# Performance work log

Measured on AMD Instinct MI355X. Metric: run time of the kernel, lower is better.

Reference implementation:

```python
import jax, jax.numpy as jnp
import numpy as np

B, L_Q, L_K, H, D = 8, 2048, 2048, 8, 64
FACTOR = 5
U_PART = max(1, min(FACTOR * int(np.ceil(np.log(L_K + 1))), L_K))  # sample_k = 40
U_TOP = max(1, min(FACTOR * int(np.ceil(np.log(L_Q + 1))), L_Q))   # n_top = 40


def setup_inputs() -> dict:
    key = jax.random.key(0)
    kq, kk, kv, ki = jax.random.split(key, 4)
    queries = jax.random.normal(kq, (B, L_Q, H, D), dtype=jnp.float32)
    keys = jax.random.normal(kk, (B, L_K, H, D), dtype=jnp.float32)
    values = jax.random.normal(kv, (B, L_K, H, D), dtype=jnp.float32)
    # random key-sampling indices (GPU randint in the torch module), shared across B,H
    index_sample = jax.random.randint(ki, (L_Q, U_PART), 0, L_K)
    return {"queries": queries, "keys": keys, "values": values,
            "index_sample": index_sample}


def reference(queries, keys, values, index_sample):
    b, l_q, h, d = queries.shape
    l_k = keys.shape[1]
    # [B, L, H, D] -> [B, H, L, D]
    Q = jnp.transpose(queries, (0, 2, 1, 3))
    K = jnp.transpose(keys, (0, 2, 1, 3))
    V = jnp.transpose(values, (0, 2, 1, 3))

    # --- _prob_QK: sparse sampling + sparsity-measure topk query selection ---
    K_sample = K[:, :, index_sample, :]                     # [B,H,L_Q,S,D]
    Q_K_sample = jnp.einsum('bhqe,bhqse->bhqs', Q, K_sample)
    M = Q_K_sample.max(axis=-1) - Q_K_sample.mean(axis=-1)  # [B,H,L_Q]
    _, M_top = jax.lax.top_k(M, U_TOP)                      # [B,H,u] query indices
    Q_reduce = jnp.take_along_axis(Q, M_top[..., None], axis=2)  # [B,H,u,D]
    scores = jnp.einsum('bhue,bhke->bhuk', Q_reduce, K)     # [B,H,u,L_K]
    scores = scores * (1.0 / np.sqrt(d))

    # --- causal mask for selected queries (mask_flag=True) ---
    key_pos = jnp.arange(l_k)
    causal = key_pos[None, None, None, :] > M_top[..., None]  # key > query pos
    scores = jnp.where(causal, -jnp.inf, scores)

    attn = jax.nn.softmax(scores, axis=-1)                  # dropout in eval mode
    attn_out = jnp.einsum('bhuk,bhkd->bhud', attn, V)       # [B,H,u,D]

    # --- initial context (causal => cumulative sum of V) + scatter update ---
    context = jnp.cumsum(V, axis=2)                         # [B,H,L_Q,D]
    b_idx = jnp.arange(b)[:, None, None]
    h_idx = jnp.arange(h)[None, :, None]
    context = context.at[b_idx, h_idx, M_top].set(attn_out)

    return jnp.transpose(context, (0, 2, 1, 3))             # [B,L_Q,H,D]
```

## Files before the change

### kernel.cpp

```cpp
#include <hip/hip_runtime.h>
#include <math.h>

#define Bb 8
#define Hh 8
#define LQ 2048
#define LK 2048
#define Dd 64
#define Uu 40
#define NCH 64
#define CHUNK (LK / NCH)
#define NSPL 8
#define CK (LK / NSPL)
#define SM_BLOCKS (Bb * (LQ / 8))
#define PART_BLOCKS (Bb * NCH / 2)
#define ATTN_BLOCKS (Bb * Hh * NSPL)
#define SCAN_BLOCKS (Bb * NCH / 2)

typedef float f32x4 __attribute__((ext_vector_type(4)));
typedef short bf16x8 __attribute__((ext_vector_type(8)));

__device__ __forceinline__ short f2bf(float x) {
    unsigned u = __float_as_uint(x);
    unsigned r = u + 0x7fffu + ((u >> 16) & 1u);
    return (short)(r >> 16);
}

__device__ __forceinline__ bf16x8 pack8(float4 a, float4 b) {
    bf16x8 r;
    r[0] = f2bf(a.x); r[1] = f2bf(a.y); r[2] = f2bf(a.z); r[3] = f2bf(a.w);
    r[4] = f2bf(b.x); r[5] = f2bf(b.y); r[6] = f2bf(b.z); r[7] = f2bf(b.w);
    return r;
}

__global__ __launch_bounds__(256) void k_main(
    const float* __restrict__ Qp, const float* __restrict__ Kp,
    const int* __restrict__ idxs, const float* __restrict__ Vp,
    float* __restrict__ M, float* __restrict__ part)
{
    int t = threadIdx.x;

    if (blockIdx.x >= SM_BLOCKS) {
        int bid2 = blockIdx.x - SM_BLOCKS;
        int b = bid2 >> 5;
        int c = (bid2 & 31) * 2 + (t >> 7);
        int h = (t >> 4) & 7, d4 = (t & 15) * 4;

        const float* vb = Vp + ((size_t)(b * LK + c * CHUNK)) * 512 + h * 64 + d4;
        float4 s = make_float4(0.f, 0.f, 0.f, 0.f);
#pragma unroll 4
        for (int l = 0; l < CHUNK; ++l) {
            float4 v = *reinterpret_cast<const float4*>(vb + (size_t)l * 512);
            s.x += v.x; s.y += v.y; s.z += v.z; s.w += v.w;
        }
        int bh = b * 8 + h;
        *reinterpret_cast<float4*>(&part[(size_t)(bh * NCH + c) * Dd + d4]) = s;
        return;
    }

    int b  = blockIdx.x & 7;
    int qt = blockIdx.x >> 3;
    int lane = t & 63, wave = t >> 6;

    __shared__ int sIdx[8 * Uu];
    for (int i = t; i < 8 * Uu; i += 256)
        sIdx[i] = idxs[(qt * 8) * Uu + i];
    __syncthreads();

    const size_t HD = 512;
    const float* Kb = Kp + (size_t)b * LK * HD + lane * 4;

#pragma unroll
    for (int i = 0; i < 2; ++i) {
        int lq = wave * 2 + i;
        int q  = qt * 8 + lq;
        const int* sI = &sIdx[lq * Uu];
#pragma unroll
        for (int ph = 0; ph < 2; ++ph) {
            f32x4 qa = __builtin_nontemporal_load(
                reinterpret_cast<const f32x4*>(
                    Qp + ((size_t)b * LQ + q) * HD + ph * 256) + lane);

            float mx = -INFINITY, sm = 0.f;
#pragma unroll 8
            for (int s = 0; s < Uu; ++s) {
                int kidx = sI[s];
                f32x4 kv = *reinterpret_cast<const f32x4*>(
                    Kb + (size_t)kidx * HD + ph * 256);
                float p = qa[0] * kv[0] + qa[1] * kv[1]
                        + qa[2] * kv[2] + qa[3] * kv[3];
                p += __shfl_xor(p, 1, 64);
                p += __shfl_xor(p, 2, 64);
                p += __shfl_xor(p, 4, 64);
                p += __shfl_xor(p, 8, 64);
                mx = fmaxf(mx, p); sm += p;
            }
            if ((lane & 15) == 0) {
                int h = ph * 4 + (lane >> 4);
                __builtin_nontemporal_store(
                    mx - sm * (1.0f / Uu), &M[((b * 8 + h) << 11) + q]);
            }
        }
    }
}

__global__ __launch_bounds__(64) void k_topk(
    const float* __restrict__ M, int* __restrict__ Mtop)
{
    int bh = blockIdx.x;
    int lane = threadIdx.x;
    __shared__ float Ml[LQ];

    for (int j = lane; j < LQ; j += 64)
        Ml[j] = M[bh * LQ + j];
    __syncthreads();

    float lv = -INFINITY; int li = LQ;
    for (int j = 0; j < 32; ++j) {
        int idx = lane + 64 * j;
        float x = Ml[idx];
        if (x > lv) { lv = x; li = idx; }
    }

    int myp = 0;
    for (int u = 0; u < Uu; ++u) {
        float v = lv; int id = li;
#pragma unroll
        for (int off = 32; off > 0; off >>= 1) {
            float ov = __shfl_xor(v, off, 64);
            int   oi = __shfl_xor(id, off, 64);
            if (ov > v || (ov == v && oi < id)) { v = ov; id = oi; }
        }
        if (u == lane) myp = id;
        if ((id & 63) == lane) {
            Ml[id] = -INFINITY;
            lv = -INFINITY; li = LQ;
            for (int j = 0; j < 32; ++j) {
                int idx = lane + 64 * j;
                float x = Ml[idx];
                if (x > lv) { lv = x; li = idx; }
            }
        }
    }

    int rank = 0;
    for (int j = 0; j < Uu; ++j) {
        int pj = __shfl(myp, j, 64);
        rank += (pj < myp && lane < Uu) ? 1 : 0;
    }
    if (lane < Uu) Mtop[bh * Uu + rank] = myp;
}

__global__ __launch_bounds__(256) void k_attn_scan(
    const float* __restrict__ Qp, const float* __restrict__ Kp,
    const float* __restrict__ Vp, const int* __restrict__ Mtop,
    const float* __restrict__ part, float* __restrict__ pacc,
    float* __restrict__ pl, float* __restrict__ out)
{
    int t = threadIdx.x;

    if (blockIdx.x >= ATTN_BLOCKS) {
        int bid2 = blockIdx.x - ATTN_BLOCKS;
        int b = bid2 >> 5;
        int ch = (bid2 & 31) * 2 + (t >> 7);
        int t2 = t & 127;
        int h = t2 >> 4, d4 = (t2 & 15) * 4;
        int bh = b * 8 + h;

        float4 run = make_float4(0.f, 0.f, 0.f, 0.f);
        for (int cc = 0; cc < ch; ++cc) {
            float4 p4 = *reinterpret_cast<const float4*>(
                &part[(size_t)(bh * NCH + cc) * Dd + d4]);
            run.x += p4.x; run.y += p4.y; run.z += p4.z; run.w += p4.w;
        }

        int l0 = ch * CHUNK;
        const float* vb = Vp + ((size_t)(b * LK + l0)) * 512 + h * 64 + d4;
        float* ob = out + ((size_t)(b * LQ + l0)) * 512 + h * 64 + d4;
#pragma unroll 4
        for (int l = 0; l < CHUNK; ++l) {
            float4 v = *reinterpret_cast<const float4*>(vb + (size_t)l * 512);
            run.x += v.x; run.y += v.y; run.z += v.z; run.w += v.w;
            *reinterpret_cast<float4*>(ob + (size_t)l * 512) = run;
        }
        return;
    }

    int bh = blockIdx.x >> 3;
    int c  = blockIdx.x & (NSPL - 1);
    int b = bh >> 3, h = bh & 7;
    int lane = t & 63, w = t >> 6;
    int col = lane & 15, hi = lane >> 4;

    __shared__ int sP[48];
    __shared__ __align__(16) short sPl[2][48][80];
    __shared__ float sL[4][48];

    if (t < 48) sP[t] = (t < Uu) ? Mtop[bh * Uu + t] : -1;
    __syncthreads();

    const int pmax = sP[Uu - 1];
    const int qmax0 = sP[15], qmax1 = sP[31];

    bf16x8 qf[3][2];
#pragma unroll
    for (int qb = 0; qb < 3; ++qb) {
        int q = qb * 16 + col;
        int row = sP[q];
#pragma unroll
        for (int ks = 0; ks < 2; ++ks) {
            const float* qp = Qp + (((size_t)b * LQ + max(row, 0)) * Hh + h) * Dd
                              + ks * 32 + hi * 8;
            float4 x = *reinterpret_cast<const float4*>(qp);
            float4 y = *reinterpret_cast<const float4*>(qp + 4);
            bf16x8 f = pack8(x, y);
            if (row < 0) f = (bf16x8)(short)0;
            qf[qb][ks] = f;
        }
    }

    f32x4 oacc[3];
    float lsum[3];
#pragma unroll
    for (int qb = 0; qb < 3; ++qb) { oacc[qb] = (f32x4)0.f; lsum[qb] = 0.f; }

    for (int tt = 0; tt < CK / 64; ++tt) {
        int k0 = c * CK + tt * 64;
        if (pmax < k0) break;
        int pb = tt & 1;
        int qblo = (k0 <= qmax0) ? 0 : ((k0 <= qmax1) ? 1 : 2);

        bf16x8 af[2];
#pragma unroll
        for (int ks = 0; ks < 2; ++ks) {
            const float* kp = Kp + (((size_t)b * LK + k0 + 16 * w + col) * Hh + h) * Dd
                              + ks * 32 + hi * 8;
            float4 x = *reinterpret_cast<const float4*>(kp);
            float4 y = *reinterpret_cast<const float4*>(kp + 4);
            af[ks] = pack8(x, y);
        }

#pragma unroll
        for (int qb = 0; qb < 3; ++qb) {
            if (qb < qblo) continue;
            f32x4 s = (f32x4)0.f;
            s = __builtin_amdgcn_mfma_f32_16x16x32_bf16(af[0], qf[qb][0], s, 0, 0, 0);
            s = __builtin_amdgcn_mfma_f32_16x16x32_bf16(af[1], qf[qb][1], s, 0, 0, 0);

            int p = sP[qb * 16 + col];
            int kbase = k0 + 16 * w + hi * 4;
            float e0 = (kbase + 0 <= p) ? __expf(s[0] * 0.125f) : 0.f;
            float e1 = (kbase + 1 <= p) ? __expf(s[1] * 0.125f) : 0.f;
            float e2 = (kbase + 2 <= p) ? __expf(s[2] * 0.125f) : 0.f;
            float e3 = (kbase + 3 <= p) ? __expf(s[3] * 0.125f) : 0.f;
            lsum[qb] += (e0 + e1) + (e2 + e3);

            int q = qb * 16 + col;
            int kl = 16 * w + hi * 4;
            unsigned p01 = (unsigned)(unsigned short)f2bf(e0)
                         | ((unsigned)(unsigned short)f2bf(e1) << 16);
            unsigned p23 = (unsigned)(unsigned short)f2bf(e2)
                         | ((unsigned)(unsigned short)f2bf(e3) << 16);
            *reinterpret_cast<unsigned*>(&sPl[pb][q][kl])     = p01;
            *reinterpret_cast<unsigned*>(&sPl[pb][q][kl + 2]) = p23;
        }
        __syncthreads();

#pragma unroll
        for (int ks = 0; ks < 2; ++ks) {
            const float* vb = Vp + (((size_t)b * LK + k0 + ks * 32 + hi * 8) * Hh + h) * Dd
                              + 16 * w + col;
            float4 x, y;
            x.x = vb[0];       x.y = vb[512];      x.z = vb[1024];     x.w = vb[1536];
            y.x = vb[2048];    y.y = vb[2560];     y.z = vb[3072];     y.w = vb[3584];
            bf16x8 vf = pack8(x, y);
#pragma unroll
            for (int qb = 0; qb < 3; ++qb) {
                if (qb < qblo) continue;
                bf16x8 pf = *reinterpret_cast<const bf16x8*>(
                    &sPl[pb][qb * 16 + col][ks * 32 + hi * 8]);
                oacc[qb] = __builtin_amdgcn_mfma_f32_16x16x32_bf16(pf, vf, oacc[qb], 0, 0, 0);
            }
        }
    }

#pragma unroll
    for (int qb = 0; qb < 3; ++qb) {
#pragma unroll
        for (int r = 0; r < 4; ++r) {
            int q = qb * 16 + hi * 4 + r;
            if (q < Uu)
                pacc[(((size_t)bh * NSPL + c) * Uu + q) * Dd + 16 * w + col] = oacc[qb][r];
        }
        lsum[qb] += __shfl_xor(lsum[qb], 16, 64);
        lsum[qb] += __shfl_xor(lsum[qb], 32, 64);
        if (lane < 16) sL[w][qb * 16 + lane] = lsum[qb];
    }
    __syncthreads();
    if (t < Uu)
        pl[((size_t)bh * NSPL + c) * Uu + t] =
            sL[0][t] + sL[1][t] + sL[2][t] + sL[3][t];
}

__global__ __launch_bounds__(256) void k_fixup(
    const int* __restrict__ Mtop, const float* __restrict__ pacc,
    const float* __restrict__ pl, float* __restrict__ out)
{
    int gid = blockIdx.x * 4 + (threadIdx.x >> 6);
    int lane = threadIdx.x & 63;
    int bh = gid / Uu, u = gid % Uu;
    int b = bh >> 3, h = bh & 7;
    int p = Mtop[bh * Uu + u];

    float A = 0.f, L = 0.f;
#pragma unroll
    for (int cc = 0; cc < NSPL; ++cc) {
        A += pacc[(((size_t)bh * NSPL + cc) * Uu + u) * Dd + lane];
        L += pl[((size_t)bh * NSPL + cc) * Uu + u];
    }
    out[(((size_t)b * LQ + p) * Hh + h) * Dd + lane] = A / L;
}

extern "C" void kernel_launch(void* const* d_in, const int* in_sizes, int n_in,
                              void* d_out, int out_size, void* d_ws, size_t ws_size,
                              hipStream_t stream) {
    const float* Qp   = (const float*)d_in[0];
    const float* Kp   = (const float*)d_in[1];
    const float* Vp   = (const float*)d_in[2];
    const int*   idxs = (const int*)d_in[3];
    float* out = (float*)d_out;

    char* w = (char*)d_ws;
    float* M    = (float*)(w);
    int*   Mtop = (int*)  (w + 512 * 1024);
    float* part = (float*)(w + 528 * 1024);
    float* pacc = (float*)(w + 1552 * 1024);
    float* pl   = (float*)(w + 6672 * 1024);

    k_main<<<SM_BLOCKS + PART_BLOCKS, 256, 0, stream>>>(Qp, Kp, idxs, Vp, M, part);
    k_topk<<<Bb * Hh, 64, 0, stream>>>(M, Mtop);
    k_attn_scan<<<ATTN_BLOCKS + SCAN_BLOCKS, 256, 0, stream>>>(
        Qp, Kp, Vp, Mtop, part, pacc, pl, out);
    k_fixup<<<Bb * Hh * Uu / 4, 256, 0, stream>>>(Mtop, pacc, pl, out);
}
```

Before: 151.6 us.

## Move cumsum scan alongside topk and fold fixup into attention via last-block counter

Moves the cumulative-sum scan blocks out of the attention kernel into the top-k kernel, so the scan runs concurrently with the serial top-k selection. The separate fixup kernel is removed: each attention split block bumps an atomic counter per (b,h), and the last one to finish merges the partial accumulators and writes the selected rows. This cuts one kernel launch and overlaps the scan with top-k. The cost is threadfence/atomic overhead and a serial merge tail in the last block of each (b,h). Correctness also depends on the scan writes landing before the attention writes, which the stream order between the two launches provides.

```diff
diff --git a/kernel.cpp b/kernel.cpp
--- a/kernel.cpp
+++ b/kernel.cpp
@@ -103,88 +103,92 @@
     }
 }
 
-__global__ __launch_bounds__(64) void k_topk(
-    const float* __restrict__ M, int* __restrict__ Mtop)
+__global__ __launch_bounds__(256) void k_topk_scan(
+    const float* __restrict__ M, int* __restrict__ Mtop,
+    const float* __restrict__ Vp, const float* __restrict__ part,
+    float* __restrict__ out, unsigned* __restrict__ cnt)
 {
-    int bh = blockIdx.x;
-    int lane = threadIdx.x;
-    __shared__ float Ml[LQ];
-
-    for (int j = lane; j < LQ; j += 64)
-        Ml[j] = M[bh * LQ + j];
-    __syncthreads();
-
-    float lv = -INFINITY; int li = LQ;
-    for (int j = 0; j < 32; ++j) {
-        int idx = lane + 64 * j;
-        float x = Ml[idx];
-        if (x > lv) { lv = x; li = idx; }
-    }
-
-    int myp = 0;
-    for (int u = 0; u < Uu; ++u) {
-        float v = lv; int id = li;
-#pragma unroll
-        for (int off = 32; off > 0; off >>= 1) {
-            float ov = __shfl_xor(v, off, 64);
-            int   oi = __shfl_xor(id, off, 64);
-            if (ov > v || (ov == v && oi < id)) { v = ov; id = oi; }
-        }
-        if (u == lane) myp = id;
-        if ((id & 63) == lane) {
-            Ml[id] = -INFINITY;
-            lv = -INFINITY; li = LQ;
-            for (int j = 0; j < 32; ++j) {
-                int idx = lane + 64 * j;
-                float x = Ml[idx];
-                if (x > lv) { lv = x; li = idx; }
-            }
-        }
-    }
-
-    int rank = 0;
-    for (int j = 0; j < Uu; ++j) {
-        int pj = __shfl(myp, j, 64);
-        rank += (pj < myp && lane < Uu) ? 1 : 0;
-    }
-    if (lane < Uu) Mtop[bh * Uu + rank] = myp;
-}
-
-__global__ __launch_bounds__(256) void k_attn_scan(
+    int t = threadIdx.x;
+
+    if (blockIdx.x < Bb * Hh) {
+        int bh = blockIdx.x;
+        if (t == 0) cnt[bh] = 0;
+        __shared__ float Ml[LQ];
+        for (int j = t; j < LQ; j += 256)
+            Ml[j] = M[bh * LQ + j];
+        __syncthreads();
+        if (t >= 64) return;
+        int lane = t;
+
+        float lv = -INFINITY; int li = LQ;
+        for (int j = 0; j < 32; ++j) {
+            int idx = lane + 64 * j;
+            float x = Ml[idx];
+            if (x > lv) { lv = x; li = idx; }
+        }
+
+        int myp = 0;
+        for (int u = 0; u < Uu; ++u) {
+            float v = lv; int id = li;
+#pragma unroll
+            for (int off = 32; off > 0; off >>= 1) {
+                float ov = __shfl_xor(v, off, 64);
+                int   oi = __shfl_xor(id, off, 64);
+                if (ov > v || (ov == v && oi < id)) { v = ov; id = oi; }
+            }
+            if (u == lane) myp = id;
+            if ((id & 63) == lane) {
+                Ml[id] = -INFINITY;
+                lv = -INFINITY; li = LQ;
+                for (int j = 0; j < 32; ++j) {
+                    int idx = lane + 64 * j;
+                    float x = Ml[idx];
+                    if (x > lv) { lv = x; li = idx; }
+                }
+            }
+        }
+
+        int rank = 0;
+        for (int j = 0; j < Uu; ++j) {
+            int pj = __shfl(myp, j, 64);
+            rank += (pj < myp && lane < Uu) ? 1 : 0;
+        }
+        if (lane < Uu) Mtop[bh * Uu + rank] = myp;
+        return;
+    }
+
+    int bid2 = blockIdx.x - Bb * Hh;
+    int b = bid2 >> 5;
+    int ch = (bid2 & 31) * 2 + (t >> 7);
+    int t2 = t & 127;
+    int h = t2 >> 4, d4 = (t2 & 15) * 4;
+    int bh = b * 8 + h;
+
+    float4 run = make_float4(0.f, 0.f, 0.f, 0.f);
+    for (int cc = 0; cc < ch; ++cc) {
+        float4 p4 = *reinterpret_cast<const float4*>(
+            &part[(size_t)(bh * NCH + cc) * Dd + d4]);
+        run.x += p4.x; run.y += p4.y; run.z += p4.z; run.w += p4.w;
+    }
+
+    int l0 = ch * CHUNK;
+    const float* vb = Vp + ((size_t)(b * LK + l0)) * 512 + h * 64 + d4;
+    float* ob = out + ((size_t)(b * LQ + l0)) * 512 + h * 64 + d4;
+#pragma unroll 4
+    for (int l = 0; l < CHUNK; ++l) {
+        float4 v = *reinterpret_cast<const float4*>(vb + (size_t)l * 512);
+        run.x += v.x; run.y += v.y; run.z += v.z; run.w += v.w;
+        *reinterpret_cast<float4*>(ob + (size_t)l * 512) = run;
+    }
+}
+
+__global__ __launch_bounds__(256) void k_attn_fixup(
     const float* __restrict__ Qp, const float* __restrict__ Kp,
     const float* __restrict__ Vp, const int* __restrict__ Mtop,
-    const float* __restrict__ part, float* __restrict__ pacc,
-    float* __restrict__ pl, float* __restrict__ out)
+    float* __restrict__ pacc, float* __restrict__ pl,
+    unsigned* __restrict__ cnt, float* __restrict__ out)
 {
     int t = threadIdx.x;
-
-    if (blockIdx.x >= ATTN_BLOCKS) {
-        int bid2 = blockIdx.x - ATTN_BLOCKS;
-        int b = bid2 >> 5;
-        int ch = (bid2 & 31) * 2 + (t >> 7);
-        int t2 = t & 127;
-        int h = t2 >> 4, d4 = (t2 & 15) * 4;
-        int bh = b * 8 + h;
-
-        float4 run = make_float4(0.f, 0.f, 0.f, 0.f);
-        for (int cc = 0; cc < ch; ++cc) {
-            float4 p4 = *reinterpret_cast<const float4*>(
-                &part[(size_t)(bh * NCH + cc) * Dd + d4]);
-            run.x += p4.x; run.y += p4.y; run.z += p4.z; run.w += p4.w;
-        }
-
-        int l0 = ch * CHUNK;
-        const float* vb = Vp + ((size_t)(b * LK + l0)) * 512 + h * 64 + d4;
-        float* ob = out + ((size_t)(b * LQ + l0)) * 512 + h * 64 + d4;
-#pragma unroll 4
-        for (int l = 0; l < CHUNK; ++l) {
-            float4 v = *reinterpret_cast<const float4*>(vb + (size_t)l * 512);
-            run.x += v.x; run.y += v.y; run.z += v.z; run.w += v.w;
-            *reinterpret_cast<float4*>(ob + (size_t)l * 512) = run;
-        }
-        return;
-    }
-
     int bh = blockIdx.x >> 3;
     int c  = blockIdx.x & (NSPL - 1);
     int b = bh >> 3, h = bh & 7;
@@ -194,6 +198,7 @@
     __shared__ int sP[48];
     __shared__ __align__(16) short sPl[2][48][80];
     __shared__ float sL[4][48];
+    __shared__ int isLast;
 
     if (t < 48) sP[t] = (t < Uu) ? Mtop[bh * Uu + t] : -1;
     __syncthreads();
@@ -299,25 +304,26 @@
     if (t < Uu)
         pl[((size_t)bh * NSPL + c) * Uu + t] =
             sL[0][t] + sL[1][t] + sL[2][t] + sL[3][t];
-}
-
-__global__ __launch_bounds__(256) void k_fixup(
-    const int* __restrict__ Mtop, const float* __restrict__ pacc,
-    const float* __restrict__ pl, float* __restrict__ out)
-{
-    int gid = blockIdx.x * 4 + (threadIdx.x >> 6);
-    int lane = threadIdx.x & 63;
-    int bh = gid / Uu, u = gid % Uu;
-    int b = bh >> 3, h = bh & 7;
-    int p = Mtop[bh * Uu + u];
-
-    float A = 0.f, L = 0.f;
-#pragma unroll
-    for (int cc = 0; cc < NSPL; ++cc) {
-        A += pacc[(((size_t)bh * NSPL + cc) * Uu + u) * Dd + lane];
-        L += pl[((size_t)bh * NSPL + cc) * Uu + u];
-    }
-    out[(((size_t)b * LQ + p) * Hh + h) * Dd + lane] = A / L;
+
+    __threadfence();
+    __syncthreads();
+    if (t == 0) isLast = (atomicAdd(&cnt[bh], 1u) == NSPL - 1) ? 1 : 0;
+    __syncthreads();
+    if (!isLast) return;
+    __threadfence();
+
+#pragma unroll
+    for (int uu = 0; uu < Uu / 4; ++uu) {
+        int u = w * (Uu / 4) + uu;
+        float A = 0.f, L = 0.f;
+#pragma unroll
+        for (int cc = 0; cc < NSPL; ++cc) {
+            A += pacc[(((size_t)bh * NSPL + cc) * Uu + u) * Dd + lane];
+            L += pl[((size_t)bh * NSPL + cc) * Uu + u];
+        }
+        int p = sP[u];
+        out[(((size_t)b * LQ + p) * Hh + h) * Dd + lane] = A / L;
+    }
 }
 
 extern "C" void kernel_launch(void* const* d_in, const int* in_sizes, int n_in,
@@ -330,15 +336,14 @@
     float* out = (float*)d_out;
 
     char* w = (char*)d_ws;
-    float* M    = (float*)(w);
-    int*   Mtop = (int*)  (w + 512 * 1024);
-    float* part = (float*)(w + 528 * 1024);
-    float* pacc = (float*)(w + 1552 * 1024);
-    float* pl   = (float*)(w + 6672 * 1024);
+    float*    M    = (float*)(w);
+    int*      Mtop = (int*)  (w + 512 * 1024);
+    float*    part = (float*)(w + 528 * 1024);
+    float*    pacc = (float*)(w + 1552 * 1024);
+    float*    pl   = (float*)(w + 6672 * 1024);
+    unsigned* cnt  = (unsigned*)(w + 6752 * 1024);
 
     k_main<<<SM_BLOCKS + PART_BLOCKS, 256, 0, stream>>>(Qp, Kp, idxs, Vp, M, part);
-    k_topk<<<Bb * Hh, 64, 0, stream>>>(M, Mtop);
-    k_attn_scan<<<ATTN_BLOCKS + SCAN_BLOCKS, 256, 0, stream>>>(
-        Qp, Kp, Vp, Mtop, part, pacc, pl, out);
-    k_fixup<<<Bb * Hh * Uu / 4, 256, 0, stream>>>(Mtop, pacc, pl, out);
-}
+    k_topk_scan<<<Bb * Hh + SCAN_BLOCKS, 256, 0, stream>>>(M, Mtop, Vp, part, out, cnt);
+    k_attn_fixup<<<ATTN_BLOCKS, 256, 0, stream>>>(Qp, Kp, Vp, Mtop, pacc, pl, cnt, out);
+}
```

Measured after the change: 207.1 us. 36.6% more time.

## Move cumsum scan into topk kernel, interleave attention key tiles, prefetch V

Applied to the files above, without the earlier changes.

The cumulative-sum scan blocks now share a launch with the top-k selection blocks, so the scan runs alongside the serial top-k instead of alongside attention. The attention kernel becomes a separate launch and spreads its 64-key tiles across splits in an interleaved way (tile c + 8*j), which balances the causal early exit across blocks. It also issues the V loads before the score MFMA and the barrier so their latency is hidden. The cost is one more dependency boundary between scan/top-k and attention, and more registers held for the prefetched V.

```diff
diff --git a/kernel.cpp b/kernel.cpp
--- a/kernel.cpp
+++ b/kernel.cpp
@@ -103,88 +103,90 @@
     }
 }
 
-__global__ __launch_bounds__(64) void k_topk(
-    const float* __restrict__ M, int* __restrict__ Mtop)
+__global__ __launch_bounds__(256) void k_topk_scan(
+    const float* __restrict__ M, int* __restrict__ Mtop,
+    const float* __restrict__ Vp, const float* __restrict__ part,
+    float* __restrict__ out)
 {
-    int bh = blockIdx.x;
-    int lane = threadIdx.x;
-    __shared__ float Ml[LQ];
-
-    for (int j = lane; j < LQ; j += 64)
-        Ml[j] = M[bh * LQ + j];
-    __syncthreads();
-
-    float lv = -INFINITY; int li = LQ;
-    for (int j = 0; j < 32; ++j) {
-        int idx = lane + 64 * j;
-        float x = Ml[idx];
-        if (x > lv) { lv = x; li = idx; }
-    }
-
-    int myp = 0;
-    for (int u = 0; u < Uu; ++u) {
-        float v = lv; int id = li;
-#pragma unroll
-        for (int off = 32; off > 0; off >>= 1) {
-            float ov = __shfl_xor(v, off, 64);
-            int   oi = __shfl_xor(id, off, 64);
-            if (ov > v || (ov == v && oi < id)) { v = ov; id = oi; }
-        }
-        if (u == lane) myp = id;
-        if ((id & 63) == lane) {
-            Ml[id] = -INFINITY;
-            lv = -INFINITY; li = LQ;
-            for (int j = 0; j < 32; ++j) {
-                int idx = lane + 64 * j;
-                float x = Ml[idx];
-                if (x > lv) { lv = x; li = idx; }
-            }
-        }
-    }
-
-    int rank = 0;
-    for (int j = 0; j < Uu; ++j) {
-        int pj = __shfl(myp, j, 64);
-        rank += (pj < myp && lane < Uu) ? 1 : 0;
-    }
-    if (lane < Uu) Mtop[bh * Uu + rank] = myp;
-}
-
-__global__ __launch_bounds__(256) void k_attn_scan(
+    int t = threadIdx.x;
+
+    if (blockIdx.x < Bb * Hh) {
+        int bh = blockIdx.x;
+        __shared__ float Ml[LQ];
+        for (int j = t; j < LQ; j += 256)
+            Ml[j] = M[bh * LQ + j];
+        __syncthreads();
+        if (t >= 64) return;
+        int lane = t;
+
+        float lv = -INFINITY; int li = LQ;
+        for (int j = 0; j < 32; ++j) {
+            int idx = lane + 64 * j;
+            float x = Ml[idx];
+            if (x > lv) { lv = x; li = idx; }
+        }
+
+        int myp = 0;
+        for (int u = 0; u < Uu; ++u) {
+            float v = lv; int id = li;
+#pragma unroll
+            for (int off = 32; off > 0; off >>= 1) {
+                float ov = __shfl_xor(v, off, 64);
+                int   oi = __shfl_xor(id, off, 64);
+                if (ov > v || (ov == v && oi < id)) { v = ov; id = oi; }
+            }
+            if (u == lane) myp = id;
+            if ((id & 63) == lane) {
+                Ml[id] = -INFINITY;
+                lv = -INFINITY; li = LQ;
+                for (int j = 0; j < 32; ++j) {
+                    int idx = lane + 64 * j;
+                    float x = Ml[idx];
+                    if (x > lv) { lv = x; li = idx; }
+                }
+            }
+        }
+
+        int rank = 0;
+        for (int j = 0; j < Uu; ++j) {
+            int pj = __shfl(myp, j, 64);
+            rank += (pj < myp && lane < Uu) ? 1 : 0;
+        }
+        if (lane < Uu) Mtop[bh * Uu + rank] = myp;
+        return;
+    }
+
+    int bid2 = blockIdx.x - Bb * Hh;
+    int b = bid2 >> 5;
+    int ch = (bid2 & 31) * 2 + (t >> 7);
+    int t2 = t & 127;
+    int h = t2 >> 4, d4 = (t2 & 15) * 4;
+    int bh = b * 8 + h;
+
+    float4 run = make_float4(0.f, 0.f, 0.f, 0.f);
+    for (int cc = 0; cc < ch; ++cc) {
+        float4 p4 = *reinterpret_cast<const float4*>(
+            &part[(size_t)(bh * NCH + cc) * Dd + d4]);
+        run.x += p4.x; run.y += p4.y; run.z += p4.z; run.w += p4.w;
+    }
+
+    int l0 = ch * CHUNK;
+    const float* vb = Vp + ((size_t)(b * LK + l0)) * 512 + h * 64 + d4;
+    float* ob = out + ((size_t)(b * LQ + l0)) * 512 + h * 64 + d4;
+#pragma unroll 4
+    for (int l = 0; l < CHUNK; ++l) {
+        float4 v = *reinterpret_cast<const float4*>(vb + (size_t)l * 512);
+        run.x += v.x; run.y += v.y; run.z += v.z; run.w += v.w;
+        *reinterpret_cast<float4*>(ob + (size_t)l * 512) = run;
+    }
+}
+
+__global__ __launch_bounds__(256) void k_attn(
     const float* __restrict__ Qp, const float* __restrict__ Kp,
     const float* __restrict__ Vp, const int* __restrict__ Mtop,
-    const float* __restrict__ part, float* __restrict__ pacc,
-    float* __restrict__ pl, float* __restrict__ out)
+    float* __restrict__ pacc, float* __restrict__ pl)
 {
     int t = threadIdx.x;
-
-    if (blockIdx.x >= ATTN_BLOCKS) {
-        int bid2 = blockIdx.x - ATTN_BLOCKS;
-        int b = bid2 >> 5;
-        int ch = (bid2 & 31) * 2 + (t >> 7);
-        int t2 = t & 127;
-        int h = t2 >> 4, d4 = (t2 & 15) * 4;
-        int bh = b * 8 + h;
-
-        float4 run = make_float4(0.f, 0.f, 0.f, 0.f);
-        for (int cc = 0; cc < ch; ++cc) {
-            float4 p4 = *reinterpret_cast<const float4*>(
-                &part[(size_t)(bh * NCH + cc) * Dd + d4]);
-            run.x += p4.x; run.y += p4.y; run.z += p4.z; run.w += p4.w;
-        }
-
-        int l0 = ch * CHUNK;
-        const float* vb = Vp + ((size_t)(b * LK + l0)) * 512 + h * 64 + d4;
-        float* ob = out + ((size_t)(b * LQ + l0)) * 512 + h * 64 + d4;
-#pragma unroll 4
-        for (int l = 0; l < CHUNK; ++l) {
-            float4 v = *reinterpret_cast<const float4*>(vb + (size_t)l * 512);
-            run.x += v.x; run.y += v.y; run.z += v.z; run.w += v.w;
-            *reinterpret_cast<float4*>(ob + (size_t)l * 512) = run;
-        }
-        return;
-    }
-
     int bh = blockIdx.x >> 3;
     int c  = blockIdx.x & (NSPL - 1);
     int b = bh >> 3, h = bh & 7;
@@ -223,10 +225,11 @@
 #pragma unroll
     for (int qb = 0; qb < 3; ++qb) { oacc[qb] = (f32x4)0.f; lsum[qb] = 0.f; }
 
-    for (int tt = 0; tt < CK / 64; ++tt) {
-        int k0 = c * CK + tt * 64;
-        if (pmax < k0) break;
-        int pb = tt & 1;
+#pragma unroll 1
+    for (int j = 0; j < LK / 64 / NSPL; ++j) {
+        int k0 = (c + NSPL * j) * 64;
+        if (k0 > pmax) break;
+        int pb = j & 1;
         int qblo = (k0 <= qmax0) ? 0 : ((k0 <= qmax1) ? 1 : 2);
 
         bf16x8 af[2];
@@ -237,6 +240,16 @@
             float4 x = *reinterpret_cast<const float4*>(kp);
             float4 y = *reinterpret_cast<const float4*>(kp + 4);
             af[ks] = pack8(x, y);
+        }
+
+        float vx[2][8];
+#pragma unroll
+        for (int ks = 0; ks < 2; ++ks) {
+            const float* vb = Vp + (((size_t)b * LK + k0 + ks * 32 + hi * 8) * Hh + h) * Dd
+                              + 16 * w + col;
+#pragma unroll
+            for (int jj = 0; jj < 8; ++jj)
+                vx[ks][jj] = vb[(size_t)jj * 512];
         }
 
 #pragma unroll
@@ -267,11 +280,8 @@
 
 #pragma unroll
         for (int ks = 0; ks < 2; ++ks) {
-            const float* vb = Vp + (((size_t)b * LK + k0 + ks * 32 + hi * 8) * Hh + h) * Dd
-                              + 16 * w + col;
-            float4 x, y;
-            x.x = vb[0];       x.y = vb[512];      x.z = vb[1024];     x.w = vb[1536];
-            y.x = vb[2048];    y.y = vb[2560];     y.z = vb[3072];     y.w = vb[3584];
+            float4 x = make_float4(vx[ks][0], vx[ks][1], vx[ks][2], vx[ks][3]);
+            float4 y = make_float4(vx[ks][4], vx[ks][5], vx[ks][6], vx[ks][7]);
             bf16x8 vf = pack8(x, y);
 #pragma unroll
             for (int qb = 0; qb < 3; ++qb) {
@@ -337,8 +347,7 @@
     float* pl   = (float*)(w + 6672 * 1024);
 
     k_main<<<SM_BLOCKS + PART_BLOCKS, 256, 0, stream>>>(Qp, Kp, idxs, Vp, M, part);
-    k_topk<<<Bb * Hh, 64, 0, stream>>>(M, Mtop);
-    k_attn_scan<<<ATTN_BLOCKS + SCAN_BLOCKS, 256, 0, stream>>>(
-        Qp, Kp, Vp, Mtop, part, pacc, pl, out);
+    k_topk_scan<<<Bb * Hh + SCAN_BLOCKS, 256, 0, stream>>>(M, Mtop, Vp, part, out);
+    k_attn<<<ATTN_BLOCKS, 256, 0, stream>>>(Qp, Kp, Vp, Mtop, pacc, pl);
     k_fixup<<<Bb * Hh * Uu / 4, 256, 0, stream>>>(Mtop, pacc, pl, out);
 }
```

Result: faster. 137.7 us (-9.2%).

## Interleave attention key splits and register-prefetch K/V tiles; widen topk load

Applied to the files above, without the earlier changes.

The attention kernel now gives each split-block strided 64-key tiles (c + 8*j) instead of a contiguous range of keys. This balances causal work across splits, since selected queries tend to have large positions. K and V for the next tile are loaded into a double-buffered register struct before the current tile's MFMAs, hiding global load latency. The top-k kernel uses 256 threads to fill shared memory before a single wave does the selection. The cost is higher register pressure from the prefetch buffers, which may reduce occupancy.

```diff
diff --git a/kernel.cpp b/kernel.cpp
--- a/kernel.cpp
+++ b/kernel.cpp
@@ -10,7 +10,6 @@
 #define NCH 64
 #define CHUNK (LK / NCH)
 #define NSPL 8
-#define CK (LK / NSPL)
 #define SM_BLOCKS (Bb * (LQ / 8))
 #define PART_BLOCKS (Bb * NCH / 2)
 #define ATTN_BLOCKS (Bb * Hh * NSPL)
@@ -103,16 +102,17 @@
     }
 }
 
-__global__ __launch_bounds__(64) void k_topk(
+__global__ __launch_bounds__(256) void k_topk(
     const float* __restrict__ M, int* __restrict__ Mtop)
 {
     int bh = blockIdx.x;
-    int lane = threadIdx.x;
+    int t = threadIdx.x;
     __shared__ float Ml[LQ];
-
-    for (int j = lane; j < LQ; j += 64)
+    for (int j = t; j < LQ; j += 256)
         Ml[j] = M[bh * LQ + j];
     __syncthreads();
+    if (t >= 64) return;
+    int lane = t;
 
     float lv = -INFINITY; int li = LQ;
     for (int j = 0; j < 32; ++j) {
@@ -150,6 +150,28 @@
     if (lane < Uu) Mtop[bh * Uu + rank] = myp;
 }
 
+struct RawTile {
+    float4 kx0, ky0, kx1, ky1;
+    float v0[8], v1[8];
+};
+
+__device__ __forceinline__ void load_tile(
+    RawTile& r, const float* __restrict__ Kp, const float* __restrict__ Vp,
+    int b, int h, int k0, int w, int col, int hi)
+{
+    const float* kp0 = Kp + (((size_t)b * LK + k0 + 16 * w + col) * Hh + h) * Dd + hi * 8;
+    r.kx0 = *reinterpret_cast<const float4*>(kp0);
+    r.ky0 = *reinterpret_cast<const float4*>(kp0 + 4);
+    r.kx1 = *reinterpret_cast<const float4*>(kp0 + 32);
+    r.ky1 = *reinterpret_cast<const float4*>(kp0 + 36);
+    const float* vb0 = Vp + (((size_t)b * LK + k0 + hi * 8) * Hh + h) * Dd + 16 * w + col;
+#pragma unroll
+    for (int jj = 0; jj < 8; ++jj) {
+        r.v0[jj] = vb0[(size_t)jj * 512];
+        r.v1[jj] = vb0[(size_t)(jj + 32) * 512];
+    }
+}
+
 __global__ __launch_bounds__(256) void k_attn_scan(
     const float* __restrict__ Qp, const float* __restrict__ Kp,
     const float* __restrict__ Vp, const int* __restrict__ Mtop,
@@ -223,28 +245,36 @@
 #pragma unroll
     for (int qb = 0; qb < 3; ++qb) { oacc[qb] = (f32x4)0.f; lsum[qb] = 0.f; }
 
-    for (int tt = 0; tt < CK / 64; ++tt) {
-        int k0 = c * CK + tt * 64;
-        if (pmax < k0) break;
-        int pb = tt & 1;
+    RawTile rb[2];
+    load_tile(rb[0], Kp, Vp, b, h, c * 64, w, col, hi);
+
+#pragma unroll
+    for (int j = 0; j < 4; ++j) {
+        int k0 = (c + NSPL * j) * 64;
+        if (k0 > pmax) break;
         int qblo = (k0 <= qmax0) ? 0 : ((k0 <= qmax1) ? 1 : 2);
 
-        bf16x8 af[2];
-#pragma unroll
-        for (int ks = 0; ks < 2; ++ks) {
-            const float* kp = Kp + (((size_t)b * LK + k0 + 16 * w + col) * Hh + h) * Dd
-                              + ks * 32 + hi * 8;
-            float4 x = *reinterpret_cast<const float4*>(kp);
-            float4 y = *reinterpret_cast<const float4*>(kp + 4);
-            af[ks] = pack8(x, y);
+        bf16x8 af0 = pack8(rb[j & 1].kx0, rb[j & 1].ky0);
+        bf16x8 af1 = pack8(rb[j & 1].kx1, rb[j & 1].ky1);
+        bf16x8 vf0 = pack8(
+            make_float4(rb[j & 1].v0[0], rb[j & 1].v0[1], rb[j & 1].v0[2], rb[j & 1].v0[3]),
+            make_float4(rb[j & 1].v0[4], rb[j & 1].v0[5], rb[j & 1].v0[6], rb[j & 1].v0[7]));
+        bf16x8 vf1 = pack8(
+            make_float4(rb[j & 1].v1[0], rb[j & 1].v1[1], rb[j & 1].v1[2], rb[j & 1].v1[3]),
+            make_float4(rb[j & 1].v1[4], rb[j & 1].v1[5], rb[j & 1].v1[6], rb[j & 1].v1[7]));
+
+        if (j < 3) {
+            int k0n = k0 + NSPL * 64;
+            if (k0n <= pmax)
+                load_tile(rb[(j + 1) & 1], Kp, Vp, b, h, k0n, w, col, hi);
         }
 
 #pragma unroll
         for (int qb = 0; qb < 3; ++qb) {
             if (qb < qblo) continue;
             f32x4 s = (f32x4)0.f;
-            s = __builtin_amdgcn_mfma_f32_16x16x32_bf16(af[0], qf[qb][0], s, 0, 0, 0);
-            s = __builtin_amdgcn_mfma_f32_16x16x32_bf16(af[1], qf[qb][1], s, 0, 0, 0);
+            s = __builtin_amdgcn_mfma_f32_16x16x32_bf16(af0, qf[qb][0], s, 0, 0, 0);
+            s = __builtin_amdgcn_mfma_f32_16x16x32_bf16(af1, qf[qb][1], s, 0, 0, 0);
 
             int p = sP[qb * 16 + col];
             int kbase = k0 + 16 * w + hi * 4;
@@ -260,26 +290,18 @@
                          | ((unsigned)(unsigned short)f2bf(e1) << 16);
             unsigned p23 = (unsigned)(unsigned short)f2bf(e2)
                          | ((unsigned)(unsigned short)f2bf(e3) << 16);
-            *reinterpret_cast<unsigned*>(&sPl[pb][q][kl])     = p01;
-            *reinterpret_cast<unsigned*>(&sPl[pb][q][kl + 2]) = p23;
+            *reinterpret_cast<unsigned*>(&sPl[j & 1][q][kl])     = p01;
+            *reinterpret_cast<unsigned*>(&sPl[j & 1][q][kl + 2]) = p23;
         }
         __syncthreads();
 
 #pragma unroll
-        for (int ks = 0; ks < 2; ++ks) {
-            const float* vb = Vp + (((size_t)b * LK + k0 + ks * 32 + hi * 8) * Hh + h) * Dd
-                              + 16 * w + col;
-            float4 x, y;
-            x.x = vb[0];       x.y = vb[512];      x.z = vb[1024];     x.w = vb[1536];
-            y.x = vb[2048];    y.y = vb[2560];     y.z = vb[3072];     y.w = vb[3584];
-            bf16x8 vf = pack8(x, y);
-#pragma unroll
-            for (int qb = 0; qb < 3; ++qb) {
-                if (qb < qblo) continue;
-                bf16x8 pf = *reinterpret_cast<const bf16x8*>(
-                    &sPl[pb][qb * 16 + col][ks * 32 + hi * 8]);
-                oacc[qb] = __builtin_amdgcn_mfma_f32_16x16x32_bf16(pf, vf, oacc[qb], 0, 0, 0);
-            }
+        for (int qb = 0; qb < 3; ++qb) {
+            if (qb < qblo) continue;
+            bf16x8 pf0 = *reinterpret_cast<const bf16x8*>(&sPl[j & 1][qb * 16 + col][hi * 8]);
+            bf16x8 pf1 = *reinterpret_cast<const bf16x8*>(&sPl[j & 1][qb * 16 + col][32 + hi * 8]);
+            oacc[qb] = __builtin_amdgcn_mfma_f32_16x16x32_bf16(pf0, vf0, oacc[qb], 0, 0, 0);
+            oacc[qb] = __builtin_amdgcn_mfma_f32_16x16x32_bf16(pf1, vf1, oacc[qb], 0, 0, 0);
         }
     }
 
@@ -337,7 +359,7 @@
     float* pl   = (float*)(w + 6672 * 1024);
 
     k_main<<<SM_BLOCKS + PART_BLOCKS, 256, 0, stream>>>(Qp, Kp, idxs, Vp, M, part);
-    k_topk<<<Bb * Hh, 64, 0, stream>>>(M, Mtop);
+    k_topk<<<Bb * Hh, 256, 0, stream>>>(M, Mtop);
     k_attn_scan<<<ATTN_BLOCKS + SCAN_BLOCKS, 256, 0, stream>>>(
         Qp, Kp, Vp, Mtop, part, pacc, pl, out);
     k_fixup<<<Bb * Hh * Uu / 4, 256, 0, stream>>>(Mtop, pacc, pl, out);
```

Result: slower. 154.7 us (+2.1%).
